# Kernel optimization log

Measured on AMD Instinct MI355X. Metric: run time of the kernel, lower is better.

## Reference

```python
import jax, jax.numpy as jnp
import numpy as np
import math

B, T, C = 4, 2048, 1024
N_HEADS = 16
D_HEAD = C // N_HEADS


def _rope_tables(d_head, max_seq_len):
    half = d_head // 2
    theta = 1.0 / (10000.0 ** (jnp.arange(half, dtype=jnp.float32) / half))
    pos = jnp.arange(max_seq_len, dtype=jnp.float32)
    freqs = jnp.outer(pos, theta)  # [S, half]
    cos = jnp.concatenate([jnp.cos(freqs), jnp.cos(freqs)], axis=-1)  # [S, d_head]
    sin = jnp.concatenate([jnp.sin(freqs), jnp.sin(freqs)], axis=-1)
    return cos, sin


def _rotate_half(x):
    d = x.shape[-1] // 2
    return jnp.concatenate([-x[..., d:], x[..., :d]], axis=-1)


def _apply_rope(x, cos, sin):
    # x: [B, H, T, d_head]; cos/sin: [T, d_head] broadcast over B,H
    return x * cos[None, None] + _rotate_half(x) * sin[None, None]


def setup_inputs() -> dict:
    key = jax.random.key(0)
    k1, k2, k3 = jax.random.split(key, 3)
    x = jax.random.normal(k1, (B, T, C), dtype=jnp.float32)
    W_qkv = jax.random.normal(k2, (C, 3 * C), dtype=jnp.float32) * (1.0 / math.sqrt(C))
    W_proj = jax.random.normal(k3, (C, C), dtype=jnp.float32) * (1.0 / math.sqrt(C))
    return {"x": x, "W_qkv": W_qkv, "W_proj": W_proj}


def reference(x, W_qkv, W_proj):
    b, t, c = x.shape
    qkv = x @ W_qkv  # [B, T, 3C]
    q, k, v = jnp.split(qkv, 3, axis=-1)

    def reshape(z):
        return z.reshape(b, t, N_HEADS, D_HEAD).transpose(0, 2, 1, 3)  # [B,H,T,dh]

    q, k, v = reshape(q), reshape(k), reshape(v)

    cos, sin = _rope_tables(D_HEAD, t)
    q = _apply_rope(q, cos, sin)
    k = _apply_rope(k, cos, sin)

    scale = 1.0 / math.sqrt(D_HEAD)
    att = jnp.einsum('bhqd,bhkd->bhqk', q, k) * scale  # [B,H,T,T]
    causal = jnp.tril(jnp.ones((t, t), dtype=bool))
    att = jnp.where(causal[None, None], att, -jnp.inf)
    att = jax.nn.softmax(att, axis=-1)
    out = jnp.einsum('bhqk,bhkd->bhqd', att, v)  # [B,H,T,dh]
    out = out.transpose(0, 2, 1, 3).reshape(b, t, c)
    return out @ W_proj
```

## Files before the change

### kernel.cpp

```cpp
#include <hip/hip_runtime.h>
#include <stdint.h>

#define Bz 4
#define Tz 2048
#define Cz 1024
#define NHz 16
#define DHz 64
#define Mz (Bz*Tz)

typedef unsigned short u16;
typedef __attribute__((ext_vector_type(8))) short short8;
typedef __attribute__((ext_vector_type(8))) unsigned short ushort8v;
typedef __attribute__((ext_vector_type(4))) unsigned short u16x4;
typedef __attribute__((ext_vector_type(4))) float f32x4;
typedef __attribute__((ext_vector_type(2))) unsigned int uint2v;

__device__ __forceinline__ float bf2f(u16 u){
  union { unsigned int i; float f; } v; v.i = ((unsigned int)u) << 16; return v.f;
}
__device__ __forceinline__ u16 f2bf(float f){
  union { float f; unsigned int i; } v; v.f = f;
  unsigned int r = v.i + 0x7FFFu + ((v.i >> 16) & 1u);
  return (u16)(r >> 16);
}


__global__ void k_cast_bf16(const float* __restrict__ in, u16* __restrict__ out, int n4){
  int i = blockIdx.x*256 + threadIdx.x;
  if (i >= n4) return;
  float4 v = ((const float4*)in)[i];
  u16x4 o;
  o[0] = f2bf(v.x); o[1] = f2bf(v.y); o[2] = f2bf(v.z); o[3] = f2bf(v.w);
  *(u16x4*)(out + (size_t)i*4) = o;
}

__global__ void k_transpose_cast(const float* __restrict__ W, u16* __restrict__ Wt, int K, int N){
  __shared__ float tile[32][33];
  int n0 = blockIdx.x*32, k0 = blockIdx.y*32;
  int tx = threadIdx.x, ty = threadIdx.y;
  #pragma unroll
  for (int i = 0; i < 32; i += 8)
    tile[ty+i][tx] = W[(size_t)(k0+ty+i)*N + n0 + tx];
  __syncthreads();
  #pragma unroll
  for (int i = 0; i < 32; i += 8)
    Wt[(size_t)(n0+ty+i)*K + k0 + tx] = f2bf(tile[tx][ty+i]);
}

__global__ void k_rope_tables(float* __restrict__ cosT, float* __restrict__ sinT){
  int idx = blockIdx.x*256 + threadIdx.x;
  int t = idx >> 5, i = idx & 31;
  float theta = exp2f(-(float)i * (13.287712379549449f / 32.0f));
  float ang = (float)t * theta;
  cosT[idx] = cosf(ang);
  sinT[idx] = sinf(ang);
}

#define GLDS(src, dstE) __builtin_amdgcn_global_load_lds( \
    (const __attribute__((address_space(1))) unsigned int*)(src), \
    (__attribute__((address_space(3))) unsigned int*)((u16*)lds + (dstE)), 16, 0, 0)

template<int Nn, int Kk, bool ROPE>
__global__ __launch_bounds__(256, 4) void k_gemmdb(const u16* __restrict__ A, const u16* __restrict__ Bt,
                        void* __restrict__ Cout, u16* __restrict__ vTout,
                        const float* __restrict__ cosT, const float* __restrict__ sinT){
  __shared__ u16 lds[2][16384];
  constexpr int NT = Kk/64;
  const int bm = blockIdx.x, bn = blockIdx.y;
  const int tid = threadIdx.x, lane = tid & 63, w = tid >> 6;
  const int wm = (w >> 1)*64, wn = (w & 1)*64;
  const int g = lane >> 4, r = lane & 15;

  const int srow8 = lane >> 3;
  const int sslot = (lane & 7) ^ srow8;
  const u16* asrc = A  + (size_t)(bm*128 + w*32 + srow8)*Kk + sslot*8;
  const u16* bsrc = Bt + (size_t)(bn*128 + w*32 + srow8)*Kk + sslot*8;
  const int dA = w*2048 + lane*8;
  const int dB = 8192 + w*2048 + lane*8;

  int a_off[4][2], b_off[4][2];
  #pragma unroll
  for (int i = 0; i < 4; ++i)
    #pragma unroll
    for (int kc = 0; kc < 2; ++kc){
      int row = wm + i*16 + r;
      a_off[i][kc] = (row*128 + kc*64 + g*16) ^ ((r & 7) << 4);
      int rowb = wn + i*16 + r;
      b_off[i][kc] = 16384 + ((rowb*128 + kc*64 + g*16) ^ ((r & 7) << 4));
    }

  f32x4 acc[4][4] = {};

#define STG(t, bi) do{ \
    const size_t ko_ = (size_t)(t)*64; \
    const int be_ = (bi)*16384; \
    GLDS(asrc + ko_,                 be_ + dA);        \
    GLDS(asrc + ko_ +  8*(size_t)Kk, be_ + dA + 512);  \
    GLDS(asrc + ko_ + 16*(size_t)Kk, be_ + dA + 1024); \
    GLDS(asrc + ko_ + 24*(size_t)Kk, be_ + dA + 1536); \
    GLDS(bsrc + ko_,                 be_ + dB);        \
    GLDS(bsrc + ko_ +  8*(size_t)Kk, be_ + dB + 512);  \
    GLDS(bsrc + ko_ + 16*(size_t)Kk, be_ + dB + 1024); \
    GLDS(bsrc + ko_ + 24*(size_t)Kk, be_ + dB + 1536); \
  }while(0)

  STG(0, 0);
  asm volatile("s_waitcnt vmcnt(0)" ::: "memory");
  __builtin_amdgcn_s_barrier();

  int buf = 0;
  #pragma unroll 1
  for (int t = 0; t < NT; ++t){
    if (t + 1 < NT) STG(t+1, buf^1);
    const char* Lb = (const char*)lds + buf*32768;
    short8 af[4][2], bf[4][2];
    #pragma unroll
    for (int i = 0; i < 4; ++i)
      #pragma unroll
      for (int kc = 0; kc < 2; ++kc){
        af[i][kc] = *(const short8*)(Lb + a_off[i][kc]);
        bf[i][kc] = *(const short8*)(Lb + b_off[i][kc]);
      }
    __builtin_amdgcn_s_setprio(1);
    #pragma unroll
    for (int i = 0; i < 4; ++i)
      #pragma unroll
      for (int j = 0; j < 4; ++j){
        acc[i][j] = __builtin_amdgcn_mfma_f32_16x16x32_bf16(af[i][0], bf[j][0], acc[i][j], 0,0,0);
        acc[i][j] = __builtin_amdgcn_mfma_f32_16x16x32_bf16(af[i][1], bf[j][1], acc[i][j], 0,0,0);
      }
    __builtin_amdgcn_s_setprio(0);
    if (t + 1 < NT){
      asm volatile("s_waitcnt vmcnt(0)" ::: "memory");
      __builtin_amdgcn_s_barrier();
      buf ^= 1;
    }
  }
#undef STG

  const int nbase = bn*128 + wn;
  if (ROPE && nbase >= 2048){
    const int b = bm >> 4;
    const int h = (nbase >> 6) & 15;
    #pragma unroll
    for (int ri = 0; ri < 4; ++ri){
      const int m0 = bm*128 + wm + ri*16 + 4*g;
      const int t0 = m0 & (Tz-1);
      #pragma unroll
      for (int cj = 0; cj < 4; ++cj){
        const int d = cj*16 + r;
        u16x4 o;
        #pragma unroll
        for (int jj = 0; jj < 4; ++jj) o[jj] = f2bf(acc[ri][cj][jj]);
        *(u16x4*)(vTout + ((size_t)((b*16 + h)*64 + d))*2048 + t0) = o;
      }
    }
  } else if (ROPE){
    const float qs = (nbase < 1024) ? 0.18033688011112042f : 1.0f;
    #pragma unroll
    for (int ri = 0; ri < 4; ++ri)
      #pragma unroll
      for (int jj = 0; jj < 4; ++jj){
        const int m = bm*128 + wm + ri*16 + 4*g + jj;
        const int t = m & (Tz-1);
        #pragma unroll
        for (int cj = 0; cj < 2; ++cj){
          const int ch = cj*16 + r;
          float cv = cosT[t*32 + ch];
          float sv = sinT[t*32 + ch];
          float lo = acc[ri][cj][jj], hi = acc[ri][cj+2][jj];
          ((u16*)Cout)[(size_t)m*Nn + nbase + ch]      = f2bf((lo*cv - hi*sv)*qs);
          ((u16*)Cout)[(size_t)m*Nn + nbase + ch + 32] = f2bf((hi*cv + lo*sv)*qs);
        }
      }
  } else {
    #pragma unroll
    for (int ri = 0; ri < 4; ++ri)
      #pragma unroll
      for (int cj = 0; cj < 4; ++cj)
        #pragma unroll
        for (int jj = 0; jj < 4; ++jj){
          const size_t m = bm*128 + wm + ri*16 + 4*g + jj;
          const size_t n = (size_t)nbase + cj*16 + r;
          ((float*)Cout)[m*Nn + n] = acc[ri][cj][jj];
        }
  }
}

__global__ __launch_bounds__(512) void k_attn2(const u16* __restrict__ qkv,
                                               const u16* __restrict__ vT,
                                               u16* __restrict__ att){
  __shared__ u16 K_lds[2*4096];
  __shared__ u16 V_lds[2*4096];
  __shared__ u16 P_lds[8*16*72];

  const int bh = blockIdx.x;
  const int b = bh >> 4, h = bh & 15;
  const int qt = 15 - blockIdx.y;
  const int tid = threadIdx.x;
  const int w = tid >> 6;
  const int lane = tid & 63;
  const int g = lane >> 4;
  const int ql = lane & 15;
  u16* Pw = P_lds + w*16*72;

  const int srow  = lane >> 3;
  const int sslot = (lane & 7) ^ srow;
  const u16* ksrc = qkv + ((size_t)(b*Tz + 8*w + srow))*3072 + 1024 + h*64 + sslot*8;
  const u16* vsrc = vT  + ((size_t)bh*64 + 8*w + srow)*2048 + sslot*8;
  u16* kdst = K_lds + w*512 + lane*8;
  u16* vdst = V_lds + w*512 + lane*8;

  short8 ones;
  #pragma unroll
  for (int i = 0; i < 8; ++i) ones[i] = (short)0x3F80;

  int fofs[4][2];
  #pragma unroll
  for (int t = 0; t < 4; ++t){
    int row = 16*t + ql;
    fofs[t][0] = (row*128 + 16*g)      ^ ((row & 7) << 4);
    fofs[t][1] = (row*128 + 64 + 16*g) ^ ((row & 7) << 4);
  }

  const int qr0w = qt*128 + w*16;
  const int nt = 2*qt + 2;

  const u16* qsrc = qkv + (size_t)(b*Tz + qr0w + ql)*3072 + h*64;
  short8 qf0 = *(const short8*)(qsrc + g*8);
  short8 qf1 = *(const short8*)(qsrc + 32 + g*8);

  f32x4 acc[4] = {{0,0,0,0},{0,0,0,0},{0,0,0,0},{0,0,0,0}};
  f32x4 accl = {0,0,0,0};

  __builtin_amdgcn_global_load_lds(
    (const __attribute__((address_space(1))) unsigned int*)(ksrc),
    (__attribute__((address_space(3))) unsigned int*)(kdst), 16, 0, 0);
  __builtin_amdgcn_global_load_lds(
    (const __attribute__((address_space(1))) unsigned int*)(vsrc),
    (__attribute__((address_space(3))) unsigned int*)(vdst), 16, 0, 0);
  __syncthreads();

  #pragma unroll 2
  for (int kt = 0; kt < nt; ++kt){
    const int buf = kt & 1;
    if (kt + 1 < nt){
      __builtin_amdgcn_global_load_lds(
        (const __attribute__((address_space(1))) unsigned int*)(ksrc + (size_t)(kt+1)*64*3072),
        (__attribute__((address_space(3))) unsigned int*)(kdst + (buf^1)*4096), 16, 0, 0);
      __builtin_amdgcn_global_load_lds(
        (const __attribute__((address_space(1))) unsigned int*)(vsrc + (kt+1)*64),
        (__attribute__((address_space(3))) unsigned int*)(vdst + (buf^1)*4096), 16, 0, 0);
    }
    const char* Kb = (const char*)(K_lds + buf*4096);
    const char* Vb = (const char*)(V_lds + buf*4096);
    const int kv0 = kt*64;

    f32x4 st[4];
    __builtin_amdgcn_s_setprio(1);
    #pragma unroll
    for (int t = 0; t < 4; ++t){
      short8 kf0 = *(const short8*)(Kb + fofs[t][0]);
      short8 kf1 = *(const short8*)(Kb + fofs[t][1]);
      f32x4 z = {0,0,0,0};
      z = __builtin_amdgcn_mfma_f32_16x16x32_bf16(kf0, qf0, z, 0, 0, 0);
      z = __builtin_amdgcn_mfma_f32_16x16x32_bf16(kf1, qf1, z, 0, 0, 0);
      st[t] = z;
    }
    __builtin_amdgcn_s_setprio(0);

    if (kv0 + 63 > qr0w){
      const int qg = qr0w + ql;
      #pragma unroll
      for (int t = 0; t < 4; ++t)
        #pragma unroll
        for (int j = 0; j < 4; ++j)
          if (kv0 + 16*t + 4*g + j > qg) st[t][j] = -1e30f;
    }

    #pragma unroll
    for (int t = 0; t < 4; ++t){
      float p0, p1, p2, p3;
      asm("v_exp_f32 %0, %1" : "=v"(p0) : "v"(st[t][0]));
      asm("v_exp_f32 %0, %1" : "=v"(p1) : "v"(st[t][1]));
      asm("v_exp_f32 %0, %1" : "=v"(p2) : "v"(st[t][2]));
      asm("v_exp_f32 %0, %1" : "=v"(p3) : "v"(st[t][3]));
      unsigned int lov, hiv;
      asm("v_cvt_pk_bf16_f32 %0, %1, %2" : "=v"(lov) : "v"(p0), "v"(p1));
      asm("v_cvt_pk_bf16_f32 %0, %1, %2" : "=v"(hiv) : "v"(p2), "v"(p3));
      uint2v pv; pv[0] = lov; pv[1] = hiv;
      *(uint2v*)((char*)Pw + ql*144 + (16*t + 4*g)*2) = pv;
    }

    short8 pf0 = *(const short8*)((char*)Pw + ql*144 + 16*g);
    short8 pf1 = *(const short8*)((char*)Pw + ql*144 + 64 + 16*g);
    __builtin_amdgcn_s_setprio(1);
    accl = __builtin_amdgcn_mfma_f32_16x16x32_bf16(pf0, ones, accl, 0, 0, 0);
    accl = __builtin_amdgcn_mfma_f32_16x16x32_bf16(pf1, ones, accl, 0, 0, 0);
    #pragma unroll
    for (int dt = 0; dt < 4; ++dt){
      short8 vf0 = *(const short8*)(Vb + fofs[dt][0]);
      short8 vf1 = *(const short8*)(Vb + fofs[dt][1]);
      acc[dt] = __builtin_amdgcn_mfma_f32_16x16x32_bf16(pf0, vf0, acc[dt], 0, 0, 0);
      acc[dt] = __builtin_amdgcn_mfma_f32_16x16x32_bf16(pf1, vf1, acc[dt], 0, 0, 0);
    }
    __builtin_amdgcn_s_setprio(0);
    __syncthreads();
  }

  float lj[4];
  #pragma unroll
  for (int j = 0; j < 4; ++j) lj[j] = 1.0f / accl[j];
  #pragma unroll
  for (int dt = 0; dt < 4; ++dt)
    #pragma unroll
    for (int j = 0; j < 4; ++j)
      att[(size_t)(b*Tz + qr0w + 4*g + j)*Cz + h*64 + dt*16 + ql] = f2bf(acc[dt][j]*lj[j]);
}


extern "C" void kernel_launch(void* const* d_in, const int* in_sizes, int n_in,
                              void* d_out, int out_size, void* d_ws, size_t ws_size,
                              hipStream_t stream){
  const float* x     = (const float*)d_in[0];
  const float* Wqkv  = (const float*)d_in[1];
  const float* Wproj = (const float*)d_in[2];
  float* out = (float*)d_out;
  char* ws = (char*)d_ws;

  u16*  xb   = (u16*)(ws);
  u16*  wqt  = (u16*)(ws + 16777216);
  u16*  wpt  = (u16*)(ws + 23068672);
  u16*  qkv  = (u16*)(ws + 25165824);
  u16*  vTr  = (u16*)(ws + 75497472);
  float* cosT = (float*)(ws + 92274688);
  float* sinT = (float*)(ws + 92536832);

  k_cast_bf16<<<Mz*Cz/4/256, 256, 0, stream>>>(x, xb, Mz*Cz/4);
  k_transpose_cast<<<dim3(3072/32, 1024/32), dim3(32,8), 0, stream>>>(Wqkv, wqt, 1024, 3072);
  k_transpose_cast<<<dim3(1024/32, 1024/32), dim3(32,8), 0, stream>>>(Wproj, wpt, 1024, 1024);
  k_rope_tables<<<Tz*32/256, 256, 0, stream>>>(cosT, sinT);

  k_gemmdb<3072, 1024, true><<<dim3(Mz/128, 3072/128), 256, 0, stream>>>(
      xb, wqt, qkv, vTr, cosT, sinT);
  k_attn2<<<dim3(Bz*NHz, 16), 512, 0, stream>>>(qkv, vTr, xb);
  k_gemmdb<1024, 1024, false><<<dim3(Mz/128, 1024/128), 256, 0, stream>>>(
      xb, wpt, out, nullptr, nullptr, nullptr);
}
```

Before: 155.1 us.

## Use single-buffered BK=32 GEMM for QKV projection, keep double-buffered for output

The QKV projection GEMM moves to a new kernel with a single 16 KB LDS buffer and a K-step of 32. Each step loads a tile, syncs, computes, and syncs again, so the load and the MFMA work no longer overlap. The kernel also drops the launch-bounds occupancy hint. The smaller LDS footprint may allow more resident blocks, but it gives up the prefetch pipelining and doubles the number of barriers. The output projection keeps the original double-buffered kernel, now specialised without the RoPE path.

```diff
diff --git a/kernel.cpp b/kernel.cpp
--- a/kernel.cpp
+++ b/kernel.cpp
@@ -56,87 +56,58 @@
   sinT[idx] = sinf(ang);
 }
 
-#define GLDS(src, dstE) __builtin_amdgcn_global_load_lds( \
-    (const __attribute__((address_space(1))) unsigned int*)(src), \
-    (__attribute__((address_space(3))) unsigned int*)((u16*)lds + (dstE)), 16, 0, 0)
-
 template<int Nn, int Kk, bool ROPE>
-__global__ __launch_bounds__(256, 4) void k_gemmdb(const u16* __restrict__ A, const u16* __restrict__ Bt,
-                        void* __restrict__ Cout, u16* __restrict__ vTout,
-                        const float* __restrict__ cosT, const float* __restrict__ sinT){
-  __shared__ u16 lds[2][16384];
-  constexpr int NT = Kk/64;
+__global__ void k_gemm97(const u16* __restrict__ A, const u16* __restrict__ Bt,
+                         void* __restrict__ Cout, u16* __restrict__ vTout,
+                         const float* __restrict__ cosT, const float* __restrict__ sinT){
+  __shared__ u16 Asub[128*32];
+  __shared__ u16 Bsub[128*32];
   const int bm = blockIdx.x, bn = blockIdx.y;
   const int tid = threadIdx.x, lane = tid & 63, w = tid >> 6;
+  const int g = lane >> 4, r = lane & 15;
   const int wm = (w >> 1)*64, wn = (w & 1)*64;
-  const int g = lane >> 4, r = lane & 15;
-
-  const int srow8 = lane >> 3;
-  const int sslot = (lane & 7) ^ srow8;
-  const u16* asrc = A  + (size_t)(bm*128 + w*32 + srow8)*Kk + sslot*8;
-  const u16* bsrc = Bt + (size_t)(bn*128 + w*32 + srow8)*Kk + sslot*8;
-  const int dA = w*2048 + lane*8;
-  const int dB = 8192 + w*2048 + lane*8;
-
-  int a_off[4][2], b_off[4][2];
-  #pragma unroll
-  for (int i = 0; i < 4; ++i)
-    #pragma unroll
-    for (int kc = 0; kc < 2; ++kc){
-      int row = wm + i*16 + r;
-      a_off[i][kc] = (row*128 + kc*64 + g*16) ^ ((r & 7) << 4);
-      int rowb = wn + i*16 + r;
-      b_off[i][kc] = 16384 + ((rowb*128 + kc*64 + g*16) ^ ((r & 7) << 4));
-    }
-
   f32x4 acc[4][4] = {};
 
-#define STG(t, bi) do{ \
-    const size_t ko_ = (size_t)(t)*64; \
-    const int be_ = (bi)*16384; \
-    GLDS(asrc + ko_,                 be_ + dA);        \
-    GLDS(asrc + ko_ +  8*(size_t)Kk, be_ + dA + 512);  \
-    GLDS(asrc + ko_ + 16*(size_t)Kk, be_ + dA + 1024); \
-    GLDS(asrc + ko_ + 24*(size_t)Kk, be_ + dA + 1536); \
-    GLDS(bsrc + ko_,                 be_ + dB);        \
-    GLDS(bsrc + ko_ +  8*(size_t)Kk, be_ + dB + 512);  \
-    GLDS(bsrc + ko_ + 16*(size_t)Kk, be_ + dB + 1024); \
-    GLDS(bsrc + ko_ + 24*(size_t)Kk, be_ + dB + 1536); \
-  }while(0)
-
-  STG(0, 0);
-  asm volatile("s_waitcnt vmcnt(0)" ::: "memory");
-  __builtin_amdgcn_s_barrier();
-
-  int buf = 0;
-  #pragma unroll 1
-  for (int t = 0; t < NT; ++t){
-    if (t + 1 < NT) STG(t+1, buf^1);
-    const char* Lb = (const char*)lds + buf*32768;
-    short8 af[4][2], bf[4][2];
+  const int srow4 = lane >> 2;
+  const int sslot = (lane & 3) ^ (srow4 & 3);
+  const u16* arow = A  + (size_t)(bm*128)*Kk;
+  const u16* brow = Bt + (size_t)(bn*128)*Kk;
+
+  int a_ofs[4], b_ofs[4];
+  #pragma unroll
+  for (int i = 0; i < 4; ++i){
+    a_ofs[i] = (wm + i*16 + r)*64 + ((g ^ (r & 3)) << 4);
+    b_ofs[i] = (wn + i*16 + r)*64 + ((g ^ (r & 3)) << 4);
+  }
+
+  for (int k0 = 0; k0 < Kk; k0 += 32){
+    #pragma unroll
+    for (int ic = 0; ic < 2; ++ic){
+      int ch = w*2 + ic;
+      int row = ch*16 + srow4;
+      __builtin_amdgcn_global_load_lds(
+        (const __attribute__((address_space(1))) unsigned int*)(arow + (size_t)row*Kk + k0 + sslot*8),
+        (__attribute__((address_space(3))) unsigned int*)(Asub + ch*512 + lane*8), 16, 0, 0);
+      __builtin_amdgcn_global_load_lds(
+        (const __attribute__((address_space(1))) unsigned int*)(brow + (size_t)row*Kk + k0 + sslot*8),
+        (__attribute__((address_space(3))) unsigned int*)(Bsub + ch*512 + lane*8), 16, 0, 0);
+    }
+    __syncthreads();
+    short8 af[4], bfr[4];
+    #pragma unroll
+    for (int i = 0; i < 4; ++i){
+      af[i]  = *(const short8*)((const char*)Asub + a_ofs[i]);
+      bfr[i] = *(const short8*)((const char*)Bsub + b_ofs[i]);
+    }
+    __builtin_amdgcn_s_setprio(1);
     #pragma unroll
     for (int i = 0; i < 4; ++i)
       #pragma unroll
-      for (int kc = 0; kc < 2; ++kc){
-        af[i][kc] = *(const short8*)(Lb + a_off[i][kc]);
-        bf[i][kc] = *(const short8*)(Lb + b_off[i][kc]);
-      }
-    __builtin_amdgcn_s_setprio(1);
-    #pragma unroll
-    for (int i = 0; i < 4; ++i)
-      #pragma unroll
-      for (int j = 0; j < 4; ++j){
-        acc[i][j] = __builtin_amdgcn_mfma_f32_16x16x32_bf16(af[i][0], bf[j][0], acc[i][j], 0,0,0);
-        acc[i][j] = __builtin_amdgcn_mfma_f32_16x16x32_bf16(af[i][1], bf[j][1], acc[i][j], 0,0,0);
-      }
+      for (int j = 0; j < 4; ++j)
+        acc[i][j] = __builtin_amdgcn_mfma_f32_16x16x32_bf16(af[i], bfr[j], acc[i][j], 0, 0, 0);
     __builtin_amdgcn_s_setprio(0);
-    if (t + 1 < NT){
-      asm volatile("s_waitcnt vmcnt(0)" ::: "memory");
-      __builtin_amdgcn_s_barrier();
-      buf ^= 1;
-    }
-  }
-#undef STG
+    __syncthreads();
+  }
 
   const int nbase = bn*128 + wn;
   if (ROPE && nbase >= 2048){
@@ -187,6 +158,100 @@
   }
 }
 
+#define GLDS(src, dstE) __builtin_amdgcn_global_load_lds( \
+    (const __attribute__((address_space(1))) unsigned int*)(src), \
+    (__attribute__((address_space(3))) unsigned int*)((u16*)lds + (dstE)), 16, 0, 0)
+
+template<int Nn, int Kk>
+__global__ __launch_bounds__(256, 4) void k_gemmdb(const u16* __restrict__ A, const u16* __restrict__ Bt,
+                        float* __restrict__ Cout){
+  __shared__ u16 lds[2][16384];
+  constexpr int NT = Kk/64;
+  const int bm = blockIdx.x, bn = blockIdx.y;
+  const int tid = threadIdx.x, lane = tid & 63, w = tid >> 6;
+  const int wm = (w >> 1)*64, wn = (w & 1)*64;
+  const int g = lane >> 4, r = lane & 15;
+
+  const int srow8 = lane >> 3;
+  const int sslot = (lane & 7) ^ srow8;
+  const u16* asrc = A  + (size_t)(bm*128 + w*32 + srow8)*Kk + sslot*8;
+  const u16* bsrc = Bt + (size_t)(bn*128 + w*32 + srow8)*Kk + sslot*8;
+  const int dA = w*2048 + lane*8;
+  const int dB = 8192 + w*2048 + lane*8;
+
+  int a_off[4][2], b_off[4][2];
+  #pragma unroll
+  for (int i = 0; i < 4; ++i)
+    #pragma unroll
+    for (int kc = 0; kc < 2; ++kc){
+      int row = wm + i*16 + r;
+      a_off[i][kc] = (row*128 + kc*64 + g*16) ^ ((r & 7) << 4);
+      int rowb = wn + i*16 + r;
+      b_off[i][kc] = 16384 + ((rowb*128 + kc*64 + g*16) ^ ((r & 7) << 4));
+    }
+
+  f32x4 acc[4][4] = {};
+
+#define STG(t, bi) do{ \
+    const size_t ko_ = (size_t)(t)*64; \
+    const int be_ = (bi)*16384; \
+    GLDS(asrc + ko_,                 be_ + dA);        \
+    GLDS(asrc + ko_ +  8*(size_t)Kk, be_ + dA + 512);  \
+    GLDS(asrc + ko_ + 16*(size_t)Kk, be_ + dA + 1024); \
+    GLDS(asrc + ko_ + 24*(size_t)Kk, be_ + dA + 1536); \
+    GLDS(bsrc + ko_,                 be_ + dB);        \
+    GLDS(bsrc + ko_ +  8*(size_t)Kk, be_ + dB + 512);  \
+    GLDS(bsrc + ko_ + 16*(size_t)Kk, be_ + dB + 1024); \
+    GLDS(bsrc + ko_ + 24*(size_t)Kk, be_ + dB + 1536); \
+  }while(0)
+
+  STG(0, 0);
+  asm volatile("s_waitcnt vmcnt(0)" ::: "memory");
+  __builtin_amdgcn_s_barrier();
+
+  int buf = 0;
+  #pragma unroll 1
+  for (int t = 0; t < NT; ++t){
+    if (t + 1 < NT) STG(t+1, buf^1);
+    const char* Lb = (const char*)lds + buf*32768;
+    short8 af[4][2], bf[4][2];
+    #pragma unroll
+    for (int i = 0; i < 4; ++i)
+      #pragma unroll
+      for (int kc = 0; kc < 2; ++kc){
+        af[i][kc] = *(const short8*)(Lb + a_off[i][kc]);
+        bf[i][kc] = *(const short8*)(Lb + b_off[i][kc]);
+      }
+    __builtin_amdgcn_s_setprio(1);
+    #pragma unroll
+    for (int i = 0; i < 4; ++i)
+      #pragma unroll
+      for (int j = 0; j < 4; ++j){
+        acc[i][j] = __builtin_amdgcn_mfma_f32_16x16x32_bf16(af[i][0], bf[j][0], acc[i][j], 0,0,0);
+        acc[i][j] = __builtin_amdgcn_mfma_f32_16x16x32_bf16(af[i][1], bf[j][1], acc[i][j], 0,0,0);
+      }
+    __builtin_amdgcn_s_setprio(0);
+    if (t + 1 < NT){
+      asm volatile("s_waitcnt vmcnt(0)" ::: "memory");
+      __builtin_amdgcn_s_barrier();
+      buf ^= 1;
+    }
+  }
+#undef STG
+
+  const int nbase = bn*128 + wn;
+  #pragma unroll
+  for (int ri = 0; ri < 4; ++ri)
+    #pragma unroll
+    for (int cj = 0; cj < 4; ++cj)
+      #pragma unroll
+      for (int jj = 0; jj < 4; ++jj){
+        const size_t m = bm*128 + wm + ri*16 + 4*g + jj;
+        const size_t n = (size_t)nbase + cj*16 + r;
+        Cout[m*Nn + n] = acc[ri][cj][jj];
+      }
+}
+
 __global__ __launch_bounds__(512) void k_attn2(const u16* __restrict__ qkv,
                                                const u16* __restrict__ vT,
                                                u16* __restrict__ att){
@@ -341,9 +406,9 @@
   k_transpose_cast<<<dim3(1024/32, 1024/32), dim3(32,8), 0, stream>>>(Wproj, wpt, 1024, 1024);
   k_rope_tables<<<Tz*32/256, 256, 0, stream>>>(cosT, sinT);
 
-  k_gemmdb<3072, 1024, true><<<dim3(Mz/128, 3072/128), 256, 0, stream>>>(
+  k_gemm97<3072, 1024, true><<<dim3(Mz/128, 3072/128), 256, 0, stream>>>(
       xb, wqt, qkv, vTr, cosT, sinT);
   k_attn2<<<dim3(Bz*NHz, 16), 512, 0, stream>>>(qkv, vTr, xb);
-  k_gemmdb<1024, 1024, false><<<dim3(Mz/128, 1024/128), 256, 0, stream>>>(
-      xb, wpt, out, nullptr, nullptr, nullptr);
-}
+  k_gemmdb<1024, 1024><<<dim3(Mz/128, 1024/128), 256, 0, stream>>>(
+      xb, wpt, out);
+}
```

Result: slower. 160.3 us (+3.4%).
